# Optimization experiments

Measured on AMD Instinct MI355X. Metric: run time of the kernel, lower is better.

## Reference

```python
import jax, jax.numpy as jnp
import numpy as np

H = 50  # hidden_size
IN = 3  # input_size
OUT = 7


def _lstm_layer(x, Wih, Whh, bih, bhh):
    # x: [B, T, D]; Wih: [4H, D]; Whh: [4H, H]; biases: [4H]
    # Precompute input-side gate pre-activations once (torch adds both biases).
    xg = jnp.einsum('btd,gd->btg', x, Wih) + bih + bhh  # [B, T, 4H]
    B = x.shape[0]
    h0 = jnp.zeros((B, H), x.dtype)
    c0 = jnp.zeros((B, H), x.dtype)

    def step(carry, xt):
        h, c = carry
        gates = xt + h @ Whh.T  # [B, 4H]
        i, f, g, o = jnp.split(gates, 4, axis=-1)  # torch gate order: i,f,g,o
        i = jax.nn.sigmoid(i)
        f = jax.nn.sigmoid(f)
        g = jnp.tanh(g)
        o = jax.nn.sigmoid(o)
        c = f * c + i * g
        h = o * jnp.tanh(c)
        return (h, c), h

    (_, _), hs = jax.lax.scan(step, (h0, c0), jnp.swapaxes(xg, 0, 1))  # hs: [T, B, H]
    return jnp.swapaxes(hs, 0, 1)  # [B, T, H]


def setup_inputs() -> dict:
    key = jax.random.key(0)
    ks = jax.random.split(key, 11)
    s = 1.0 / np.sqrt(H)  # torch LSTM init scale
    B, T = 4096, 512
    return {
        'x': jax.random.normal(ks[0], (B, T, IN), jnp.float32),
        'Wih0': jax.random.uniform(ks[1], (4 * H, IN), jnp.float32, -s, s),
        'Whh0': jax.random.uniform(ks[2], (4 * H, H), jnp.float32, -s, s),
        'bih0': jax.random.uniform(ks[3], (4 * H,), jnp.float32, -s, s),
        'bhh0': jax.random.uniform(ks[4], (4 * H,), jnp.float32, -s, s),
        'Wih1': jax.random.uniform(ks[5], (4 * H, H), jnp.float32, -s, s),
        'Whh1': jax.random.uniform(ks[6], (4 * H, H), jnp.float32, -s, s),
        'bih1': jax.random.uniform(ks[7], (4 * H,), jnp.float32, -s, s),
        'bhh1': jax.random.uniform(ks[8], (4 * H,), jnp.float32, -s, s),
        'Wfc': jax.random.uniform(ks[9], (OUT, H), jnp.float32, -s, s),
        'bfc': jax.random.uniform(ks[10], (OUT,), jnp.float32, -s, s),
    }


def reference(x, Wih0, Whh0, bih0, bhh0, Wih1, Whh1, bih1, bhh1, Wfc, bfc):
    h1 = _lstm_layer(x, Wih0, Whh0, bih0, bhh0)   # [B, T, H]
    h2 = _lstm_layer(h1, Wih1, Whh1, bih1, bhh1)  # [B, T, H]
    last = h2[:, -1, :]                           # [B, H]
    return last @ Wfc.T + bfc                     # [B, 7]
```

## Files before the change

kernel.cpp:

```cpp
#include <hip/hip_runtime.h>

#define HD 50
#define TT 512
#define BRR 16
#define TC 32
#define KS 136

using f16   = _Float16;
using f16x8 = __attribute__((ext_vector_type(8))) f16;
using f32x4 = __attribute__((ext_vector_type(4))) float;

#define LOG2E 1.4426950408889634f

__device__ __forceinline__ short f2h_bits(float f) {
    f16 h = (f16)f;
    return *reinterpret_cast<short*>(&h);
}
__device__ __forceinline__ float h2f(short b) {
    f16 h = *reinterpret_cast<f16*>(&b);
    return (float)h;
}
__device__ __forceinline__ float frcp(float x) { return __builtin_amdgcn_rcpf(x); }
#if __has_builtin(__builtin_amdgcn_exp2f)
__device__ __forceinline__ float fexp2(float x) { return __builtin_amdgcn_exp2f(x); }
#else
__device__ __forceinline__ float fexp2(float x) { return exp2f(x); }
#endif

__global__ __launch_bounds__(512, 2) void lstm2_uni2(
    const float* __restrict__ x,
    const float* __restrict__ Wih0, const float* __restrict__ Whh0,
    const float* __restrict__ bih0, const float* __restrict__ bhh0,
    const float* __restrict__ Wih1, const float* __restrict__ Whh1,
    const float* __restrict__ bih1, const float* __restrict__ bhh1,
    const float* __restrict__ Wfc, const float* __restrict__ bfc,
    float* __restrict__ out)
{
    __shared__ short s_A[2][BRR][KS];
    __shared__ float s_xs[2][BRR][TC * 3];

    const int tid  = threadIdx.x;
    const int wid  = tid >> 6;
    const int lane = tid & 63;
    const int lr   = lane & 15;
    const int lq   = lane >> 4;
    const int r0   = blockIdx.x * BRR;

    const int  p     = 8 * lr + wid;
    const bool valid = (p < 100);
    const bool isL1  = valid && (p >= 50);
    const int  u     = valid ? (isL1 ? p - 50 : p) : 0;
    const int  wcol  = isL1 ? 64 + u : u;

    f16x8 bw[4][4];
    float bvT[4];
    #pragma unroll
    for (int tt = 0; tt < 4; ++tt) {
        const float sc = (tt == 2) ? (2.0f * LOG2E) : (-LOG2E);
        const int g = tt * HD + u;
        if (!isL1) {
            bvT[tt] = valid ? (bih0[g] + bhh0[g]) * sc : 0.f;
            #pragma unroll
            for (int s = 0; s < 4; ++s) {
                #pragma unroll
                for (int j = 0; j < 8; ++j) {
                    const int k = s*32 + lq*8 + j;
                    float wv = 0.f;
                    if (valid) {
                        if (k < HD) wv = Whh0[g*HD + k];
                        else if (k < HD + 3) wv = Wih0[g*3 + (k - HD)];
                    }
                    bw[tt][s][j] = (f16)(wv * sc);
                }
            }
        } else {
            bvT[tt] = (bih1[g] + bhh1[g]) * sc;
            #pragma unroll
            for (int s = 0; s < 4; ++s) {
                #pragma unroll
                for (int j = 0; j < 8; ++j) {
                    const int k = s*32 + lq*8 + j;
                    float wv = 0.f;
                    if (k < HD) wv = Wih1[g*HD + k];
                    else if (k >= 64 && k < 64 + HD) wv = Whh1[g*HD + (k - 64)];
                    bw[tt][s][j] = (f16)(wv * sc);
                }
            }
        }
    }

    float cst[4] = {0.f, 0.f, 0.f, 0.f};

    const bool xduty = (wid < 4) && (lr >= 13);
    const int  xidx  = wid * 12 + (lr - 13) * 4 + lq;
    const int  xrow  = xidx / 3, xd = xidx % 3;

    for (int q = tid; q < 2 * BRR * KS; q += 512) ((short*)s_A)[q] = 0;
    for (int q = tid; q < BRR * TC * 3; q += 512) {
        const int rr = q / (TC * 3), qq = q % (TC * 3);
        s_xs[0][rr][qq] = x[(size_t)(r0 + rr) * (TT * 3) + qq];
    }
    __syncthreads();
    if (xduty) s_A[0][xrow][HD + xd] = f2h_bits(s_xs[0][xrow][xd]);
    __syncthreads();

    for (int n = 0; n <= TT; ++n) {
        const char* ab = (const char*)&s_A[n & 1][0][0];
        f16x8 a[4];
        #pragma unroll
        for (int s = 0; s < 4; ++s)
            a[s] = *(const f16x8*)(ab + lr * (2 * KS) + s * 64 + lq * 16);
        f32x4 acc[4];
        #pragma unroll
        for (int tt = 0; tt < 4; ++tt) { const float b = bvT[tt]; acc[tt] = (f32x4){b, b, b, b}; }
        #pragma unroll
        for (int s = 0; s < 4; ++s) {
            #pragma unroll
            for (int tt = 0; tt < 4; ++tt)
                acc[tt] = __builtin_amdgcn_mfma_f32_16x16x32_f16(a[s], bw[tt][s], acc[tt], 0, 0, 0);
        }

        const bool act = valid && (isL1 ? (n >= 1) : (n < TT));
        if (act) {
            #pragma unroll
            for (int j = 0; j < 4; ++j) {
                const float ei = fexp2(acc[0][j]);
                const float ef = fexp2(acc[1][j]);
                const float eg = fexp2(acc[2][j]);
                const float eo = fexp2(acc[3][j]);
                const float ig = (eg - 1.0f) * frcp((eg + 1.0f) * (1.0f + ei));
                const float fv = frcp(1.0f + ef);
                const float c  = fv * cst[j] + ig;
                cst[j] = c;
                const float ec = fexp2(c * (2.0f * LOG2E));
                const float h  = (ec - 1.0f) * frcp((ec + 1.0f) * (1.0f + eo));
                s_A[(n + 1) & 1][lq * 4 + j][wcol] = f2h_bits(h);
            }
        }
        if (xduty && (n + 1) < TT) {
            const int tn = n + 1;
            s_A[(n + 1) & 1][xrow][HD + xd] =
                f2h_bits(s_xs[(tn / TC) & 1][xrow][(tn % TC) * 3 + xd]);
        }
        {
            const int t2s = n + 2;
            if (t2s < TT && (t2s % TC) == 0) {
                const int cb = (t2s / TC) & 1;
                for (int q = tid; q < BRR * TC * 3; q += 512) {
                    const int rr = q / (TC * 3), qq = q % (TC * 3);
                    s_xs[cb][rr][qq] = x[(size_t)(r0 + rr) * (TT * 3) + (size_t)t2s * 3 + qq];
                }
            }
        }
        __syncthreads();
    }

    if (tid < BRR * 7) {
        const int r = tid / 7, o = tid % 7;
        float acc = bfc[o];
        #pragma unroll
        for (int uu = 0; uu < HD; ++uu)
            acc += h2f(s_A[1][r][64 + uu]) * Wfc[o * HD + uu];
        out[(size_t)(r0 + r) * 7 + o] = acc;
    }
}

extern "C" void kernel_launch(void* const* d_in, const int* in_sizes, int n_in,
                              void* d_out, int out_size, void* d_ws, size_t ws_size,
                              hipStream_t stream) {
    const float* xp    = (const float*)d_in[0];
    const float* Wih0  = (const float*)d_in[1];
    const float* Whh0  = (const float*)d_in[2];
    const float* bih0  = (const float*)d_in[3];
    const float* bhh0  = (const float*)d_in[4];
    const float* Wih1  = (const float*)d_in[5];
    const float* Whh1  = (const float*)d_in[6];
    const float* bih1  = (const float*)d_in[7];
    const float* bhh1  = (const float*)d_in[8];
    const float* Wfc   = (const float*)d_in[9];
    const float* bfc   = (const float*)d_in[10];
    float* outp = (float*)d_out;

    const int B = in_sizes[0] / (TT * 3);
    const int grid = B / BRR;

    lstm2_uni2<<<grid, 512, 0, stream>>>(
        xp, Wih0, Whh0, bih0, bhh0, Wih1, Whh1, bih1, bhh1, Wfc, bfc, outp);
}
```

Before: 399.1 us.

## Split layers across wave groups and run MFMA and activations in anti-phase

Assigns waves 0-3 to layer 0 and waves 4-7 to layer 1, each handling all 50 hidden units with 4 units per lane row. Each step is split into two half-phases around a barrier, so one group does its MFMAs while the other does its transcendental activations. The goal is to overlap matrix-core and VALU/SFU work and to let layer 0 use only the two K-slices it needs. This adds a second barrier per step and one extra pipeline iteration, and it leaves some lanes idle where u is 50 or more.

```diff
diff --git a/kernel.cpp b/kernel.cpp
--- a/kernel.cpp
+++ b/kernel.cpp
@@ -27,7 +27,7 @@
 __device__ __forceinline__ float fexp2(float x) { return exp2f(x); }
 #endif
 
-__global__ __launch_bounds__(512, 2) void lstm2_uni2(
+__global__ __launch_bounds__(512, 2) void lstm2_anti(
     const float* __restrict__ x,
     const float* __restrict__ Wih0, const float* __restrict__ Whh0,
     const float* __restrict__ bih0, const float* __restrict__ bhh0,
@@ -46,22 +46,24 @@
     const int lq   = lane >> 4;
     const int r0   = blockIdx.x * BRR;
 
-    const int  p     = 8 * lr + wid;
-    const bool valid = (p < 100);
-    const bool isL1  = valid && (p >= 50);
-    const int  u     = valid ? (isL1 ? p - 50 : p) : 0;
-    const int  wcol  = isL1 ? 64 + u : u;
+    const bool isS0 = (wid < 4);
+    const int  wsub = wid & 3;
+    const int  u     = 4 * lr + wsub;
+    const bool valid = (u < HD);
+    const int  wcol  = isS0 ? u : 64 + u;
 
     f16x8 bw[4][4];
     float bvT[4];
     #pragma unroll
     for (int tt = 0; tt < 4; ++tt) {
         const float sc = (tt == 2) ? (2.0f * LOG2E) : (-LOG2E);
-        const int g = tt * HD + u;
-        if (!isL1) {
+        const int g = tt * HD + (valid ? u : 0);
+        #pragma unroll
+        for (int s = 0; s < 4; ++s) bw[tt][s] = (f16x8)0;
+        if (isS0) {
             bvT[tt] = valid ? (bih0[g] + bhh0[g]) * sc : 0.f;
             #pragma unroll
-            for (int s = 0; s < 4; ++s) {
+            for (int s = 0; s < 2; ++s) {
                 #pragma unroll
                 for (int j = 0; j < 8; ++j) {
                     const int k = s*32 + lq*8 + j;
@@ -74,15 +76,17 @@
                 }
             }
         } else {
-            bvT[tt] = (bih1[g] + bhh1[g]) * sc;
+            bvT[tt] = valid ? (bih1[g] + bhh1[g]) * sc : 0.f;
             #pragma unroll
             for (int s = 0; s < 4; ++s) {
                 #pragma unroll
                 for (int j = 0; j < 8; ++j) {
                     const int k = s*32 + lq*8 + j;
                     float wv = 0.f;
-                    if (k < HD) wv = Wih1[g*HD + k];
-                    else if (k >= 64 && k < 64 + HD) wv = Whh1[g*HD + (k - 64)];
+                    if (valid) {
+                        if (k < HD) wv = Wih1[g*HD + k];
+                        else if (k >= 64 && k < 64 + HD) wv = Whh1[g*HD + (k - 64)];
+                    }
                     bw[tt][s][j] = (f16)(wv * sc);
                 }
             }
@@ -91,9 +95,17 @@
 
     float cst[4] = {0.f, 0.f, 0.f, 0.f};
 
-    const bool xduty = (wid < 4) && (lr >= 13);
-    const int  xidx  = wid * 12 + (lr - 13) * 4 + lq;
-    const int  xrow  = xidx / 3, xd = xidx % 3;
+    f32x4 acc[4];
+    #pragma unroll
+    for (int tt = 0; tt < 4; ++tt) acc[tt] = (f32x4){0, 0, 0, 0};
+
+    bool xduty = false; int xrow = 0, xd = 0;
+    if (isS0 && !valid) {
+        const int base[4]   = {0, 12, 24, 40};
+        const int lstart[4] = {13, 13, 12, 12};
+        const int xidx = base[wsub] + (lr - lstart[wsub]) * 4 + lq;
+        if (xidx < 48) { xduty = true; xrow = xidx / 3; xd = xidx % 3; }
+    }
 
     for (int q = tid; q < 2 * BRR * KS; q += 512) ((short*)s_A)[q] = 0;
     for (int q = tid; q < BRR * TC * 3; q += 512) {
@@ -104,46 +116,84 @@
     if (xduty) s_A[0][xrow][HD + xd] = f2h_bits(s_xs[0][xrow][xd]);
     __syncthreads();
 
-    for (int n = 0; n <= TT; ++n) {
-        const char* ab = (const char*)&s_A[n & 1][0][0];
-        f16x8 a[4];
-        #pragma unroll
-        for (int s = 0; s < 4; ++s)
-            a[s] = *(const f16x8*)(ab + lr * (2 * KS) + s * 64 + lq * 16);
-        f32x4 acc[4];
-        #pragma unroll
-        for (int tt = 0; tt < 4; ++tt) { const float b = bvT[tt]; acc[tt] = (f32x4){b, b, b, b}; }
-        #pragma unroll
-        for (int s = 0; s < 4; ++s) {
-            #pragma unroll
-            for (int tt = 0; tt < 4; ++tt)
-                acc[tt] = __builtin_amdgcn_mfma_f32_16x16x32_f16(a[s], bw[tt][s], acc[tt], 0, 0, 0);
-        }
-
-        const bool act = valid && (isL1 ? (n >= 1) : (n < TT));
-        if (act) {
-            #pragma unroll
-            for (int j = 0; j < 4; ++j) {
-                const float ei = fexp2(acc[0][j]);
-                const float ef = fexp2(acc[1][j]);
-                const float eg = fexp2(acc[2][j]);
-                const float eo = fexp2(acc[3][j]);
-                const float ig = (eg - 1.0f) * frcp((eg + 1.0f) * (1.0f + ei));
-                const float fv = frcp(1.0f + ef);
-                const float c  = fv * cst[j] + ig;
-                cst[j] = c;
-                const float ec = fexp2(c * (2.0f * LOG2E));
-                const float h  = (ec - 1.0f) * frcp((ec + 1.0f) * (1.0f + eo));
-                s_A[(n + 1) & 1][lq * 4 + j][wcol] = f2h_bits(h);
-            }
-        }
-        if (xduty && (n + 1) < TT) {
-            const int tn = n + 1;
-            s_A[(n + 1) & 1][xrow][HD + xd] =
-                f2h_bits(s_xs[(tn / TC) & 1][xrow][(tn % TC) * 3 + xd]);
+    for (int i = 0; i <= TT + 1; ++i) {
+        const char* ab = (const char*)&s_A[i & 1][0][0];
+
+        if (isS0) {
+            if (i < TT) {
+                f16x8 a[2];
+                #pragma unroll
+                for (int s = 0; s < 2; ++s)
+                    a[s] = *(const f16x8*)(ab + lr * (2 * KS) + s * 64 + lq * 16);
+                #pragma unroll
+                for (int tt = 0; tt < 4; ++tt) { const float b = bvT[tt]; acc[tt] = (f32x4){b, b, b, b}; }
+                #pragma unroll
+                for (int s = 0; s < 2; ++s) {
+                    #pragma unroll
+                    for (int tt = 0; tt < 4; ++tt)
+                        acc[tt] = __builtin_amdgcn_mfma_f32_16x16x32_f16(a[s], bw[tt][s], acc[tt], 0, 0, 0);
+                }
+            }
+        } else {
+            if (valid && i >= 2) {
+                #pragma unroll
+                for (int j = 0; j < 4; ++j) {
+                    const float ei = fexp2(acc[0][j]);
+                    const float ef = fexp2(acc[1][j]);
+                    const float eg = fexp2(acc[2][j]);
+                    const float eo = fexp2(acc[3][j]);
+                    const float ig = (eg - 1.0f) * frcp((eg + 1.0f) * (1.0f + ei));
+                    const float fv = frcp(1.0f + ef);
+                    const float c  = fv * cst[j] + ig;
+                    cst[j] = c;
+                    const float ec = fexp2(c * (2.0f * LOG2E));
+                    const float h  = (ec - 1.0f) * frcp((ec + 1.0f) * (1.0f + eo));
+                    s_A[i & 1][lq * 4 + j][wcol] = f2h_bits(h);
+                }
+            }
+        }
+        __syncthreads();
+
+        if (isS0) {
+            if (valid && i < TT) {
+                #pragma unroll
+                for (int j = 0; j < 4; ++j) {
+                    const float ei = fexp2(acc[0][j]);
+                    const float ef = fexp2(acc[1][j]);
+                    const float eg = fexp2(acc[2][j]);
+                    const float eo = fexp2(acc[3][j]);
+                    const float ig = (eg - 1.0f) * frcp((eg + 1.0f) * (1.0f + ei));
+                    const float fv = frcp(1.0f + ef);
+                    const float c  = fv * cst[j] + ig;
+                    cst[j] = c;
+                    const float ec = fexp2(c * (2.0f * LOG2E));
+                    const float h  = (ec - 1.0f) * frcp((ec + 1.0f) * (1.0f + eo));
+                    s_A[(i + 1) & 1][lq * 4 + j][wcol] = f2h_bits(h);
+                }
+            }
+            if (xduty && (i + 1) < TT) {
+                const int tn = i + 1;
+                s_A[(i + 1) & 1][xrow][HD + xd] =
+                    f2h_bits(s_xs[(tn / TC) & 1][xrow][(tn % TC) * 3 + xd]);
+            }
+        } else {
+            if (i >= 1 && i <= TT) {
+                f16x8 a[4];
+                #pragma unroll
+                for (int s = 0; s < 4; ++s)
+                    a[s] = *(const f16x8*)(ab + lr * (2 * KS) + s * 64 + lq * 16);
+                #pragma unroll
+                for (int tt = 0; tt < 4; ++tt) { const float b = bvT[tt]; acc[tt] = (f32x4){b, b, b, b}; }
+                #pragma unroll
+                for (int s = 0; s < 4; ++s) {
+                    #pragma unroll
+                    for (int tt = 0; tt < 4; ++tt)
+                        acc[tt] = __builtin_amdgcn_mfma_f32_16x16x32_f16(a[s], bw[tt][s], acc[tt], 0, 0, 0);
+                }
+            }
         }
         {
-            const int t2s = n + 2;
+            const int t2s = i + 2;
             if (t2s < TT && (t2s % TC) == 0) {
                 const int cb = (t2s / TC) & 1;
                 for (int q = tid; q < BRR * TC * 3; q += 512) {
@@ -157,11 +207,11 @@
 
     if (tid < BRR * 7) {
         const int r = tid / 7, o = tid % 7;
-        float acc = bfc[o];
+        float acc2 = bfc[o];
         #pragma unroll
         for (int uu = 0; uu < HD; ++uu)
-            acc += h2f(s_A[1][r][64 + uu]) * Wfc[o * HD + uu];
-        out[(size_t)(r0 + r) * 7 + o] = acc;
+            acc2 += h2f(s_A[1][r][64 + uu]) * Wfc[o * HD + uu];
+        out[(size_t)(r0 + r) * 7 + o] = acc2;
     }
 }
 
@@ -184,6 +234,6 @@
     const int B = in_sizes[0] / (TT * 3);
     const int grid = B / BRR;
 
-    lstm2_uni2<<<grid, 512, 0, stream>>>(
+    lstm2_anti<<<grid, 512, 0, stream>>>(
         xp, Wih0, Whh0, bih0, bhh0, Wih1, Whh1, bih1, bhh1, Wfc, bfc, outp);
 }
```

Measured after the change: 469.4 us. +17.6%, slower.

## Halve rows per block, make each thread compute both LSTM layers

Applied to the files above, without the earlier changes.

Blocks drop to 8 batch rows and 256 threads. Each thread now holds weights for both layers for one hidden unit and runs both MFMA sets. The 16-row MFMA tile is half padding, and lane-shuffle exchanges let each half-wave finish the activations for distinct rows. This doubles the grid and removes the 8-wave split over units, aiming for better occupancy and balance. In exchange it wastes half the MFMA work on padding rows and adds shuffles and register pressure.

```diff
diff --git a/kernel.cpp b/kernel.cpp
--- a/kernel.cpp
+++ b/kernel.cpp
@@ -2,7 +2,7 @@
 
 #define HD 50
 #define TT 512
-#define BRR 16
+#define BRR 8
 #define TC 32
 #define KS 136
 
@@ -27,7 +27,7 @@
 __device__ __forceinline__ float fexp2(float x) { return exp2f(x); }
 #endif
 
-__global__ __launch_bounds__(512, 2) void lstm2_uni2(
+__global__ __launch_bounds__(256, 2) void lstm2_dual(
     const float* __restrict__ x,
     const float* __restrict__ Wih0, const float* __restrict__ Whh0,
     const float* __restrict__ bih0, const float* __restrict__ bhh0,
@@ -36,7 +36,7 @@
     const float* __restrict__ Wfc, const float* __restrict__ bfc,
     float* __restrict__ out)
 {
-    __shared__ short s_A[2][BRR][KS];
+    __shared__ short s_A[2][16][KS];
     __shared__ float s_xs[2][BRR][TC * 3];
 
     const int tid  = threadIdx.x;
@@ -46,62 +46,67 @@
     const int lq   = lane >> 4;
     const int r0   = blockIdx.x * BRR;
 
-    const int  p     = 8 * lr + wid;
-    const bool valid = (p < 100);
-    const bool isL1  = valid && (p >= 50);
-    const int  u     = valid ? (isL1 ? p - 50 : p) : 0;
-    const int  wcol  = isL1 ? 64 + u : u;
-
-    f16x8 bw[4][4];
-    float bvT[4];
+    const int  u     = 4 * lr + wid;
+    const bool valid = (u < HD);
+    const bool hi    = (lane >= 32);
+    const int  rwb   = (lq & 1) * 4 + ((lq >> 1) & 1) * 2;
+
+    f16x8 bwA[4][2], bwB[4][4];
+    float bvA[4], bvB[4];
     #pragma unroll
     for (int tt = 0; tt < 4; ++tt) {
         const float sc = (tt == 2) ? (2.0f * LOG2E) : (-LOG2E);
-        const int g = tt * HD + u;
-        if (!isL1) {
-            bvT[tt] = valid ? (bih0[g] + bhh0[g]) * sc : 0.f;
-            #pragma unroll
-            for (int s = 0; s < 4; ++s) {
-                #pragma unroll
-                for (int j = 0; j < 8; ++j) {
-                    const int k = s*32 + lq*8 + j;
-                    float wv = 0.f;
-                    if (valid) {
-                        if (k < HD) wv = Whh0[g*HD + k];
-                        else if (k < HD + 3) wv = Wih0[g*3 + (k - HD)];
-                    }
-                    bw[tt][s][j] = (f16)(wv * sc);
+        const int g = tt * HD + (valid ? u : 0);
+        bvA[tt] = valid ? (bih0[g] + bhh0[g]) * sc : 0.f;
+        #pragma unroll
+        for (int s = 0; s < 2; ++s) {
+            #pragma unroll
+            for (int j = 0; j < 8; ++j) {
+                const int k = s * 32 + lq * 8 + j;
+                float wv = 0.f;
+                if (valid) {
+                    if (k < HD) wv = Whh0[g * HD + k];
+                    else if (k < HD + 3) wv = Wih0[g * 3 + (k - HD)];
                 }
-            }
-        } else {
-            bvT[tt] = (bih1[g] + bhh1[g]) * sc;
-            #pragma unroll
-            for (int s = 0; s < 4; ++s) {
-                #pragma unroll
-                for (int j = 0; j < 8; ++j) {
-                    const int k = s*32 + lq*8 + j;
-                    float wv = 0.f;
-                    if (k < HD) wv = Wih1[g*HD + k];
-                    else if (k >= 64 && k < 64 + HD) wv = Whh1[g*HD + (k - 64)];
-                    bw[tt][s][j] = (f16)(wv * sc);
+                bwA[tt][s][j] = (f16)(wv * sc);
+            }
+        }
+        bvB[tt] = valid ? (bih1[g] + bhh1[g]) * sc : 0.f;
+        #pragma unroll
+        for (int s = 0; s < 4; ++s) {
+            #pragma unroll
+            for (int j = 0; j < 8; ++j) {
+                const int k = s * 32 + lq * 8 + j;
+                float wv = 0.f;
+                if (valid) {
+                    if (k < HD) wv = Wih1[g * HD + k];
+                    else if (k >= 64 && k < 64 + HD) wv = Whh1[g * HD + (k - 64)];
                 }
-            }
-        }
-    }
-
-    float cst[4] = {0.f, 0.f, 0.f, 0.f};
-
-    const bool xduty = (wid < 4) && (lr >= 13);
-    const int  xidx  = wid * 12 + (lr - 13) * 4 + lq;
-    const int  xrow  = xidx / 3, xd = xidx % 3;
-
-    for (int q = tid; q < 2 * BRR * KS; q += 512) ((short*)s_A)[q] = 0;
-    for (int q = tid; q < BRR * TC * 3; q += 512) {
+                bwB[tt][s][j] = (f16)(wv * sc);
+            }
+        }
+    }
+
+    float cstA[2] = {0.f, 0.f};
+    float cstB[2] = {0.f, 0.f};
+
+    const bool xduty = (wid == 0) && (lr >= 13);
+    const int  xi    = (lr - 13) * 4 + lq;
+
+    for (int q = tid; q < 2 * 16 * KS; q += 256) ((short*)s_A)[q] = 0;
+    for (int q = tid; q < BRR * TC * 3; q += 256) {
         const int rr = q / (TC * 3), qq = q % (TC * 3);
         s_xs[0][rr][qq] = x[(size_t)(r0 + rr) * (TT * 3) + qq];
     }
     __syncthreads();
-    if (xduty) s_A[0][xrow][HD + xd] = f2h_bits(s_xs[0][xrow][xd]);
+    if (xduty) {
+        #pragma unroll
+        for (int e = 0; e < 2; ++e) {
+            const int slot = 2 * xi + e;
+            const int rr = slot / 3, dd = slot % 3;
+            s_A[0][rr][HD + dd] = f2h_bits(s_xs[0][rr][dd]);
+        }
+    }
     __syncthreads();
 
     for (int n = 0; n <= TT; ++n) {
@@ -110,43 +115,90 @@
         #pragma unroll
         for (int s = 0; s < 4; ++s)
             a[s] = *(const f16x8*)(ab + lr * (2 * KS) + s * 64 + lq * 16);
-        f32x4 acc[4];
-        #pragma unroll
-        for (int tt = 0; tt < 4; ++tt) { const float b = bvT[tt]; acc[tt] = (f32x4){b, b, b, b}; }
+
+        f32x4 accA[4], accB[4];
+        #pragma unroll
+        for (int tt = 0; tt < 4; ++tt) { const float b = bvA[tt]; accA[tt] = (f32x4){b, b, b, b}; }
+        #pragma unroll
+        for (int tt = 0; tt < 4; ++tt) { const float b = bvB[tt]; accB[tt] = (f32x4){b, b, b, b}; }
+        #pragma unroll
+        for (int s = 0; s < 2; ++s) {
+            #pragma unroll
+            for (int tt = 0; tt < 4; ++tt)
+                accA[tt] = __builtin_amdgcn_mfma_f32_16x16x32_f16(a[s], bwA[tt][s], accA[tt], 0, 0, 0);
+        }
         #pragma unroll
         for (int s = 0; s < 4; ++s) {
             #pragma unroll
             for (int tt = 0; tt < 4; ++tt)
-                acc[tt] = __builtin_amdgcn_mfma_f32_16x16x32_f16(a[s], bw[tt][s], acc[tt], 0, 0, 0);
-        }
-
-        const bool act = valid && (isL1 ? (n >= 1) : (n < TT));
-        if (act) {
-            #pragma unroll
-            for (int j = 0; j < 4; ++j) {
-                const float ei = fexp2(acc[0][j]);
-                const float ef = fexp2(acc[1][j]);
-                const float eg = fexp2(acc[2][j]);
-                const float eo = fexp2(acc[3][j]);
+                accB[tt] = __builtin_amdgcn_mfma_f32_16x16x32_f16(a[s], bwB[tt][s], accB[tt], 0, 0, 0);
+        }
+
+        float swA[4][2], swB[4][2];
+        #pragma unroll
+        for (int tt = 0; tt < 4; ++tt) {
+            #pragma unroll
+            for (int jj = 0; jj < 2; ++jj) {
+                swA[tt][jj] = __shfl_xor(accA[tt][2 + jj], 32);
+                swB[tt][jj] = __shfl_xor(accB[tt][2 + jj], 32);
+            }
+        }
+
+        if (valid && n < TT) {
+            #pragma unroll
+            for (int jj = 0; jj < 2; ++jj) {
+                const float pi = hi ? swA[0][jj] : accA[0][jj];
+                const float pf = hi ? swA[1][jj] : accA[1][jj];
+                const float pg = hi ? swA[2][jj] : accA[2][jj];
+                const float po = hi ? swA[3][jj] : accA[3][jj];
+                const float ei = fexp2(pi);
+                const float ef = fexp2(pf);
+                const float eg = fexp2(pg);
+                const float eo = fexp2(po);
                 const float ig = (eg - 1.0f) * frcp((eg + 1.0f) * (1.0f + ei));
                 const float fv = frcp(1.0f + ef);
-                const float c  = fv * cst[j] + ig;
-                cst[j] = c;
+                const float c  = fv * cstA[jj] + ig;
+                cstA[jj] = c;
                 const float ec = fexp2(c * (2.0f * LOG2E));
                 const float h  = (ec - 1.0f) * frcp((ec + 1.0f) * (1.0f + eo));
-                s_A[(n + 1) & 1][lq * 4 + j][wcol] = f2h_bits(h);
+                s_A[(n + 1) & 1][rwb + jj][u] = f2h_bits(h);
+            }
+        }
+        if (valid && n >= 1) {
+            #pragma unroll
+            for (int jj = 0; jj < 2; ++jj) {
+                const float pi = hi ? swB[0][jj] : accB[0][jj];
+                const float pf = hi ? swB[1][jj] : accB[1][jj];
+                const float pg = hi ? swB[2][jj] : accB[2][jj];
+                const float po = hi ? swB[3][jj] : accB[3][jj];
+                const float ei = fexp2(pi);
+                const float ef = fexp2(pf);
+                const float eg = fexp2(pg);
+                const float eo = fexp2(po);
+                const float ig = (eg - 1.0f) * frcp((eg + 1.0f) * (1.0f + ei));
+                const float fv = frcp(1.0f + ef);
+                const float c  = fv * cstB[jj] + ig;
+                cstB[jj] = c;
+                const float ec = fexp2(c * (2.0f * LOG2E));
+                const float h  = (ec - 1.0f) * frcp((ec + 1.0f) * (1.0f + eo));
+                s_A[(n + 1) & 1][rwb + jj][64 + u] = f2h_bits(h);
             }
         }
         if (xduty && (n + 1) < TT) {
             const int tn = n + 1;
-            s_A[(n + 1) & 1][xrow][HD + xd] =
-                f2h_bits(s_xs[(tn / TC) & 1][xrow][(tn % TC) * 3 + xd]);
+            #pragma unroll
+            for (int e = 0; e < 2; ++e) {
+                const int slot = 2 * xi + e;
+                const int rr = slot / 3, dd = slot % 3;
+                s_A[(n + 1) & 1][rr][HD + dd] =
+                    f2h_bits(s_xs[(tn / TC) & 1][rr][(tn % TC) * 3 + dd]);
+            }
         }
         {
             const int t2s = n + 2;
             if (t2s < TT && (t2s % TC) == 0) {
                 const int cb = (t2s / TC) & 1;
-                for (int q = tid; q < BRR * TC * 3; q += 512) {
+                for (int q = tid; q < BRR * TC * 3; q += 256) {
                     const int rr = q / (TC * 3), qq = q % (TC * 3);
                     s_xs[cb][rr][qq] = x[(size_t)(r0 + rr) * (TT * 3) + (size_t)t2s * 3 + qq];
                 }
@@ -184,6 +236,6 @@
     const int B = in_sizes[0] / (TT * 3);
     const int grid = B / BRR;
 
-    lstm2_uni2<<<grid, 512, 0, stream>>>(
+    lstm2_dual<<<grid, 256, 0, stream>>>(
         xp, Wih0, Whh0, bih0, bhh0, Wih1, Whh1, bih1, bhh1, Wfc, bfc, outp);
 }
```

After: 577.2 us. +44.6%, slower.

## Split LSTM gate activations across two wave groups and batch reciprocals

Applied to the files above, without the earlier changes.

Doubles the block to 1024 threads so that two groups of 8 waves each compute the same MFMA tiles. Each group then handles half of the four rows per lane in the activation stage, which cuts per-thread transcendental work. Reciprocals are merged so one rcp serves two rows (Montgomery-style), and the time loop is unrolled by 2. The cost is that the MFMA work is done twice, the per-thread register budget shrinks to fit 1024-thread blocks at 4 per CU, and barrier cost rises with more waves.

```diff
diff --git a/kernel.cpp b/kernel.cpp
--- a/kernel.cpp
+++ b/kernel.cpp
@@ -27,7 +27,7 @@
 __device__ __forceinline__ float fexp2(float x) { return exp2f(x); }
 #endif
 
-__global__ __launch_bounds__(512, 2) void lstm2_uni2(
+__global__ __launch_bounds__(1024, 4) void lstm2_tlp(
     const float* __restrict__ x,
     const float* __restrict__ Wih0, const float* __restrict__ Whh0,
     const float* __restrict__ bih0, const float* __restrict__ bhh0,
@@ -46,11 +46,14 @@
     const int lq   = lane >> 4;
     const int r0   = blockIdx.x * BRR;
 
-    const int  p     = 8 * lr + wid;
+    const int  wsub = wid & 7;
+    const bool jhi  = (wid >= 8);
+    const int  p     = 8 * lr + wsub;
     const bool valid = (p < 100);
     const bool isL1  = valid && (p >= 50);
     const int  u     = valid ? (isL1 ? p - 50 : p) : 0;
     const int  wcol  = isL1 ? 64 + u : u;
+    const int  rbase = lq * 4 + (jhi ? 2 : 0);
 
     f16x8 bw[4][4];
     float bvT[4];
@@ -89,14 +92,14 @@
         }
     }
 
-    float cst[4] = {0.f, 0.f, 0.f, 0.f};
+    float cst[2] = {0.f, 0.f};
 
     const bool xduty = (wid < 4) && (lr >= 13);
     const int  xidx  = wid * 12 + (lr - 13) * 4 + lq;
     const int  xrow  = xidx / 3, xd = xidx % 3;
 
-    for (int q = tid; q < 2 * BRR * KS; q += 512) ((short*)s_A)[q] = 0;
-    for (int q = tid; q < BRR * TC * 3; q += 512) {
+    for (int q = tid; q < 2 * BRR * KS; q += 1024) ((short*)s_A)[q] = 0;
+    for (int q = tid; q < BRR * TC * 3; q += 1024) {
         const int rr = q / (TC * 3), qq = q % (TC * 3);
         s_xs[0][rr][qq] = x[(size_t)(r0 + rr) * (TT * 3) + qq];
     }
@@ -104,6 +107,7 @@
     if (xduty) s_A[0][xrow][HD + xd] = f2h_bits(s_xs[0][xrow][xd]);
     __syncthreads();
 
+    #pragma unroll 2
     for (int n = 0; n <= TT; ++n) {
         const char* ab = (const char*)&s_A[n & 1][0][0];
         f16x8 a[4];
@@ -122,20 +126,42 @@
 
         const bool act = valid && (isL1 ? (n >= 1) : (n < TT));
         if (act) {
-            #pragma unroll
-            for (int j = 0; j < 4; ++j) {
-                const float ei = fexp2(acc[0][j]);
-                const float ef = fexp2(acc[1][j]);
-                const float eg = fexp2(acc[2][j]);
-                const float eo = fexp2(acc[3][j]);
-                const float ig = (eg - 1.0f) * frcp((eg + 1.0f) * (1.0f + ei));
-                const float fv = frcp(1.0f + ef);
-                const float c  = fv * cst[j] + ig;
-                cst[j] = c;
+            float pre[4][2];
+            #pragma unroll
+            for (int tt = 0; tt < 4; ++tt) {
+                pre[tt][0] = jhi ? acc[tt][2] : acc[tt][0];
+                pre[tt][1] = jhi ? acc[tt][3] : acc[tt][1];
+            }
+            float P[2], num1[2], D1[2], D2[2], eo2[2];
+            #pragma unroll
+            for (int jj = 0; jj < 2; ++jj) {
+                const float ei = fexp2(pre[0][jj]);
+                const float ef = fexp2(pre[1][jj]);
+                const float eg = fexp2(pre[2][jj]);
+                eo2[jj] = fexp2(pre[3][jj]);
+                D1[jj] = (eg + 1.0f) * (1.0f + ei);
+                D2[jj] = 1.0f + ef;
+                P[jj]  = D1[jj] * D2[jj];
+                num1[jj] = eg - 1.0f;
+            }
+            const float rA = frcp(P[0] * P[1]);
+            const float iP[2] = { rA * P[1], rA * P[0] };
+            float num2[2], den2[2];
+            #pragma unroll
+            for (int jj = 0; jj < 2; ++jj) {
+                const float ig = num1[jj] * (iP[jj] * D2[jj]);
+                const float fv = iP[jj] * D1[jj];
+                const float c  = fv * cst[jj] + ig;
+                cst[jj] = c;
                 const float ec = fexp2(c * (2.0f * LOG2E));
-                const float h  = (ec - 1.0f) * frcp((ec + 1.0f) * (1.0f + eo));
-                s_A[(n + 1) & 1][lq * 4 + j][wcol] = f2h_bits(h);
-            }
+                num2[jj] = ec - 1.0f;
+                den2[jj] = (ec + 1.0f) * (1.0f + eo2[jj]);
+            }
+            const float rC = frcp(den2[0] * den2[1]);
+            const float iD[2] = { rC * den2[1], rC * den2[0] };
+            #pragma unroll
+            for (int jj = 0; jj < 2; ++jj)
+                s_A[(n + 1) & 1][rbase + jj][wcol] = f2h_bits(num2[jj] * iD[jj]);
         }
         if (xduty && (n + 1) < TT) {
             const int tn = n + 1;
@@ -146,7 +172,7 @@
             const int t2s = n + 2;
             if (t2s < TT && (t2s % TC) == 0) {
                 const int cb = (t2s / TC) & 1;
-                for (int q = tid; q < BRR * TC * 3; q += 512) {
+                for (int q = tid; q < BRR * TC * 3; q += 1024) {
                     const int rr = q / (TC * 3), qq = q % (TC * 3);
                     s_xs[cb][rr][qq] = x[(size_t)(r0 + rr) * (TT * 3) + (size_t)t2s * 3 + qq];
                 }
@@ -184,6 +210,6 @@
     const int B = in_sizes[0] / (TT * 3);
     const int grid = B / BRR;
 
-    lstm2_uni2<<<grid, 512, 0, stream>>>(
+    lstm2_tlp<<<grid, 1024, 0, stream>>>(
         xp, Wih0, Whh0, bih0, bhh0, Wih1, Whh1, bih1, bhh1, Wfc, bfc, outp);
 }
```

Result: slower. 483.2 us (+21.1%).
